# Optimization experiments

Hardware: AMD Instinct MI355X
Metric: run time of the kernel (lower is better)

Reference implementation:

```python
import jax, jax.numpy as jnp
import numpy as np

B, H, W, C = 4, 64, 64, 1024
REF_FRAC = 0.05


def setup_inputs() -> dict:
    key = jax.random.key(0)
    k1, k2 = jax.random.split(key)
    embeddings = jax.random.normal(k1, (B, H, W, C), dtype=jnp.float32)
    # sparse boolean reference masks, guaranteed non-empty per item
    ref_masks = jax.random.uniform(k2, (B, H, W)) < REF_FRAC
    ref_masks = ref_masks.at[:, 0, 0].set(True)
    return {"embeddings": embeddings, "ref_masks": ref_masks}


def reference(embeddings, ref_masks):
    """Fixed-shape JAX translation of InstanceMatcher.forward_match.

    Instead of per-item argwhere/dynamic gather, we compute the full NxN
    cosine-similarity matrix and express the ref/remaining partition with
    boolean masks. Returns:
      match  : [B, N, N] bool  -- match[b, i, j] True iff patch i is a ref patch,
               patch j is a non-ref patch, and sim > per-item median threshold
               (equivalent to the rows of the original `maps_to` output; global
               flat indices i, j map to coords via (i // W, i % W)).
      sim    : [B, N, N] float -- cosine similarities (all pairs).
      thresh : [B] float       -- median-of-max threshold per item.
    """
    Bn, Hn, Wn, Cn = embeddings.shape
    N = Hn * Wn
    x = embeddings.reshape(Bn, N, Cn)
    m = ref_masks.reshape(Bn, N)  # [B, N] bool, True = ref patch

    # F.normalize(x, dim=-1): x / max(||x||, eps)
    norm = jnp.linalg.norm(x, axis=-1, keepdims=True)
    fn = x / jnp.maximum(norm, 1e-12)

    # all-pairs cosine similarity; only (ref row, non-ref col) entries are used
    sim = jnp.einsum('bnc,bmc->bnm', fn, fn)  # [B, N, N]

    valid = m[:, :, None] & (~m)[:, None, :]  # [B, N, N]

    # max over remaining (non-ref) columns, per ref row
    max_per_ref = jnp.max(jnp.where(valid, sim, -jnp.inf), axis=2)  # [B, N]

    # torch.median (lower median) over the ref rows only: sort with non-ref
    # rows pushed to +inf, then pick element (k-1)//2 where k = #ref patches
    vals = jnp.where(m, max_per_ref, jnp.inf)
    vals_sorted = jnp.sort(vals, axis=1)
    k = jnp.sum(m, axis=1)  # [B]
    med_idx = (k - 1) // 2
    thresh = jnp.take_along_axis(vals_sorted, med_idx[:, None], axis=1)[:, 0]  # [B]

    match = valid & (sim > thresh[:, None, None])
    return match, sim, thresh
```

## Files before the change

kernel.cpp:

```cpp
#include <hip/hip_runtime.h>
#include <hip/hip_bf16.h>
#include <stdint.h>
#include <math.h>

#define BQ 4
#define NQ 4096
#define CQ 1024

#define WS_CTR      0
#define WS_THRESH   64
#define WS_MASK     256
#define WS_REFIDX   17408
#define WS_MAXV     82944
#define WS_INVN     148480
#define WS_FNB      (4u << 20)
#define WS_NEED     (WS_FNB + (32u << 20) + (1u << 20))

typedef __bf16 bf16x8 __attribute__((ext_vector_type(8)));
typedef float floatx4 __attribute__((ext_vector_type(4)));

__global__ void k_detect(const uint8_t* mraw, int* ctr) {
    int c123 = 0, c3f = 0;
    for (int i = threadIdx.x; i < BQ * NQ; i += blockDim.x) {
        uint8_t v = mraw[i];
        int m4 = i & 3;
        if (m4 != 0 && v != 0) c123++;
        if (m4 == 3 && v == 0x3F) c3f++;
    }
    atomicAdd(&ctr[0], c123);
    atomicAdd(&ctr[1], c3f);
}

__global__ void k_canon(const void* mraw, const int* ctr, uint8_t* maskc) {
    int i = blockIdx.x * blockDim.x + threadIdx.x;
    if (i >= BQ * NQ) return;
    int c123 = ctr[0], c3f = ctr[1];
    uint8_t v;
    if (c3f > 64) {
        v = (((const float*)mraw)[i] != 0.0f) ? 1 : 0;
    } else if (c123 == 0) {
        v = (((const int*)mraw)[i] != 0) ? 1 : 0;
    } else {
        v = (((const uint8_t*)mraw)[i] != 0) ? 1 : 0;
    }
    maskc[i] = v;
}

__global__ void k_compact(const uint8_t* maskc, int* refCount, int* refIdx) {
    int b = blockIdx.x;
    for (int i = threadIdx.x; i < NQ; i += blockDim.x) {
        if (maskc[b * NQ + i]) {
            int p = atomicAdd(&refCount[b], 1);
            refIdx[b * NQ + p] = i;
        }
    }
}

__global__ __launch_bounds__(128) void k_prep(const float* x, double* invn, __bf16* fnb) {
    int row = blockIdx.x;
    int t = threadIdx.x;
    const float4* xr = (const float4*)(x + (long long)row * CQ);
    float4 a = xr[t * 2 + 0];
    float4 c = xr[t * 2 + 1];
    double s = (double)a.x * a.x + (double)a.y * a.y + (double)a.z * a.z + (double)a.w * a.w
             + (double)c.x * c.x + (double)c.y * c.y + (double)c.z * c.z + (double)c.w * c.w;
    __shared__ double red[128];
    __shared__ double invs;
    red[t] = s;
    __syncthreads();
    for (int o = 64; o > 0; o >>= 1) {
        if (t < o) red[t] += red[t + o];
        __syncthreads();
    }
    if (t == 0) {
        double inv = 1.0 / fmax(sqrt(red[0]), 1e-12);
        invn[row] = inv;
        invs = inv;
    }
    __syncthreads();
    float ir = (float)invs;
    bf16x8 o8;
    o8[0] = (__bf16)(a.x * ir); o8[1] = (__bf16)(a.y * ir);
    o8[2] = (__bf16)(a.z * ir); o8[3] = (__bf16)(a.w * ir);
    o8[4] = (__bf16)(c.x * ir); o8[5] = (__bf16)(c.y * ir);
    o8[6] = (__bf16)(c.z * ir); o8[7] = (__bf16)(c.w * ir);
    *(bf16x8*)(fnb + (long long)row * CQ + t * 8) = o8;
}

#define GRID_MEGA 6144
__global__ __launch_bounds__(256) void k_mega(const __bf16* fnb, const float* x,
                                              const double* invn, const int* refCount,
                                              const int* refIdx, const uint8_t* maskc,
                                              float* sim, float* match) {
    __shared__ __align__(16) char smem[16384];
    const int t = threadIdx.x;
    const int id = blockIdx.x;

    if ((id % 3) == 2) {
        const int fid = id / 3;
        const int b = fid >> 9;
        const int rowT0 = (fid >> 6) & 7;
        const int colT = fid & 63;
        const int cnt = refCount[b];
        float* sAf = (float*)smem;
        float* sBf = (float*)(smem + 4608);
        int* sRef  = (int*)(smem + 13312);
        const float* xb = x + (long long)b * NQ * CQ;
        const int lrA = t >> 3, lkA = (t & 7) * 4;
        const int lrB = t >> 2, lkB = (t & 3) * 8;
        const int ty = t >> 4, tx = t & 15;
        for (int rowT = rowT0; rowT * 32 < cnt; rowT += 8) {
            __syncthreads();
            if (t < 32) {
                int rg = rowT * 32 + t;
                sRef[t] = (rg < cnt) ? refIdx[b * NQ + rg] : refIdx[b * NQ];
            }
            __syncthreads();
            const int arow = sRef[lrA];
            const int brow = colT * 64 + lrB;
            double acc[2][4] = {};
            for (int k0 = 0; k0 < CQ; k0 += 32) {
                float4 av = *(const float4*)(xb + (long long)arow * CQ + k0 + lkA);
                float4 b0 = *(const float4*)(xb + (long long)brow * CQ + k0 + lkB);
                float4 b1 = *(const float4*)(xb + (long long)brow * CQ + k0 + lkB + 4);
                __syncthreads();
                sAf[(lkA + 0) * 36 + lrA] = av.x; sAf[(lkA + 1) * 36 + lrA] = av.y;
                sAf[(lkA + 2) * 36 + lrA] = av.z; sAf[(lkA + 3) * 36 + lrA] = av.w;
                sBf[(lkB + 0) * 68 + lrB] = b0.x; sBf[(lkB + 1) * 68 + lrB] = b0.y;
                sBf[(lkB + 2) * 68 + lrB] = b0.z; sBf[(lkB + 3) * 68 + lrB] = b0.w;
                sBf[(lkB + 4) * 68 + lrB] = b1.x; sBf[(lkB + 5) * 68 + lrB] = b1.y;
                sBf[(lkB + 6) * 68 + lrB] = b1.z; sBf[(lkB + 7) * 68 + lrB] = b1.w;
                __syncthreads();
#pragma unroll
                for (int kk = 0; kk < 32; kk++) {
                    double a0 = (double)sAf[kk * 36 + ty * 2 + 0];
                    double a1 = (double)sAf[kk * 36 + ty * 2 + 1];
                    float4 bq = *(const float4*)(sBf + kk * 68 + tx * 4);
                    double b0d = (double)bq.x, b1d = (double)bq.y;
                    double b2d = (double)bq.z, b3d = (double)bq.w;
                    acc[0][0] += a0 * b0d; acc[0][1] += a0 * b1d;
                    acc[0][2] += a0 * b2d; acc[0][3] += a0 * b3d;
                    acc[1][0] += a1 * b0d; acc[1][1] += a1 * b1d;
                    acc[1][2] += a1 * b2d; acc[1][3] += a1 * b3d;
                }
            }
#pragma unroll
            for (int i2 = 0; i2 < 2; i2++) {
                int rg = rowT * 32 + ty * 2 + i2;
                if (rg >= cnt) continue;
                int r = sRef[ty * 2 + i2];
                double ir = invn[b * NQ + r];
#pragma unroll
                for (int j2 = 0; j2 < 4; j2++) {
                    int c = colT * 64 + tx * 4 + j2;
                    double ic = invn[b * NQ + c];
                    sim[((long long)b * NQ + r) * NQ + c] = (float)(acc[i2][j2] * ir * ic);
                }
            }
        }
    } else {
        const int gid = (id / 3) * 2 + (id % 3);
        if (gid >= 2112) return;
        const int b = gid / 528;
        int rem = gid % 528;
        int rT = 0;
        while (rem >= 32 - rT) { rem -= 32 - rT; rT++; }
        const int cT = rT + rem;
        const int rowBase = rT * 128;
        const int colBase = cT * 128;
        const __bf16* base = fnb + (long long)b * NQ * CQ;
        __bf16* smA = (__bf16*)smem;
        __bf16* smB = (__bf16*)(smem + 8192);

        const int lane = threadIdx.x & 63;
        const int w = threadIdx.x >> 6;
        const int wr = w >> 1, wc = w & 1;
        const int ldrow = lane >> 2;
        const int ldcolS = ((lane & 3) * 8) ^ (((lane >> 3) & 3) << 3);
        const int co = ((lane >> 4) * 8) ^ (((lane >> 1) & 3) << 3);

        floatx4 acc[4][4] = {};

        for (int k0 = 0; k0 < CQ; k0 += 32) {
            __syncthreads();
#pragma unroll
            for (int i = 0; i < 2; i++) {
                int rsub = w * 16 + i * 64;
                const __bf16* gA = base + (long long)(rowBase + rsub + ldrow) * CQ + k0 + ldcolS;
                const __bf16* gB = base + (long long)(colBase + rsub + ldrow) * CQ + k0 + ldcolS;
                __builtin_amdgcn_global_load_lds(
                    (const __attribute__((address_space(1))) void*)gA,
                    (__attribute__((address_space(3))) void*)(smA + rsub * 32), 16, 0, 0);
                __builtin_amdgcn_global_load_lds(
                    (const __attribute__((address_space(1))) void*)gB,
                    (__attribute__((address_space(3))) void*)(smB + rsub * 32), 16, 0, 0);
            }
            __syncthreads();

            bf16x8 af[4], bfv[4];
#pragma unroll
            for (int i = 0; i < 4; i++) {
                af[i]  = *(const bf16x8*)(smA + (wr * 64 + i * 16 + (lane & 15)) * 32 + co);
                bfv[i] = *(const bf16x8*)(smB + (wc * 64 + i * 16 + (lane & 15)) * 32 + co);
            }
#pragma unroll
            for (int i = 0; i < 4; i++)
#pragma unroll
                for (int j = 0; j < 4; j++)
                    acc[i][j] = __builtin_amdgcn_mfma_f32_16x16x32_bf16(af[i], bfv[j], acc[i][j], 0, 0, 0);
        }

        float* simb = sim + (long long)b * NQ * NQ;
        float* matb = match + (long long)b * NQ * NQ;
        const uint8_t* mrow = maskc + b * NQ;
#pragma unroll
        for (int i = 0; i < 4; i++) {
            int r0 = rowBase + wr * 64 + i * 16 + (lane >> 4) * 4;
#pragma unroll
            for (int r = 0; r < 4; r++) {
                bool isRef = mrow[r0 + r] != 0;
#pragma unroll
                for (int j = 0; j < 4; j++) {
                    int c = colBase + wc * 64 + j * 16 + (lane & 15);
                    if (!isRef) simb[(long long)(r0 + r) * NQ + c] = acc[i][j][r];
                    matb[(long long)(r0 + r) * NQ + c] = 0.0f;
                }
            }
        }

        if (rT != cT) {
            floatx4 zero4 = {0.0f, 0.0f, 0.0f, 0.0f};
#pragma unroll
            for (int i = 0; i < 4; i++) {
                int r0 = rowBase + wr * 64 + i * 16 + (lane >> 4) * 4;
#pragma unroll
                for (int j = 0; j < 4; j++) {
                    int c = colBase + wc * 64 + j * 16 + (lane & 15);
                    long long off = (long long)c * NQ + r0;
                    if (!mrow[c]) *(floatx4*)(simb + off) = acc[i][j];
                    *(floatx4*)(matb + off) = zero4;
                }
            }
        }
    }
}

__global__ __launch_bounds__(256) void k_rowmax(const float* sim, const uint8_t* maskc,
                                                const int* refCount, const int* refIdx,
                                                float* maxv) {
    int b = blockIdx.y;
    int cnt = refCount[b];
    __shared__ float red[256];
    for (int slot = blockIdx.x; slot < cnt; slot += gridDim.x) {
        int row = refIdx[b * NQ + slot];
        const float* rp = sim + ((long long)b * NQ + row) * NQ;
        float mx = -INFINITY;
        for (int j = threadIdx.x; j < NQ; j += 256) {
            if (!maskc[b * NQ + j]) mx = fmaxf(mx, rp[j]);
        }
        __syncthreads();
        red[threadIdx.x] = mx;
        __syncthreads();
        for (int o = 128; o > 0; o >>= 1) {
            if (threadIdx.x < o) red[threadIdx.x] = fmaxf(red[threadIdx.x], red[threadIdx.x + o]);
            __syncthreads();
        }
        if (threadIdx.x == 0) maxv[b * NQ + slot] = red[0];
    }
}

__global__ __launch_bounds__(256) void k_median(const float* maxv, const int* refCount,
                                                float* threshv, float* outth) {
    int b = blockIdx.x;
    int k = refCount[b];
    __shared__ float vals[NQ];
    __shared__ float result;
    for (int i = threadIdx.x; i < k; i += blockDim.x) vals[i] = maxv[b * NQ + i];
    __syncthreads();
    int med = (k - 1) / 2;
    for (int t0 = threadIdx.x; t0 < k; t0 += blockDim.x) {
        float v = vals[t0];
        int cl = 0, ce = 0;
        for (int j = 0; j < k; j++) {
            float w = vals[j];
            cl += (w < v) ? 1 : 0;
            ce += (w == v) ? 1 : 0;
        }
        if (cl <= med && med < cl + ce) result = v;
    }
    __syncthreads();
    if (threadIdx.x == 0) {
        threshv[b] = result;
        outth[b] = result;
    }
}

__global__ __launch_bounds__(256) void k_match(const float* sim, const uint8_t* maskc,
                                               const int* refCount, const int* refIdx,
                                               const float* threshv, float* match) {
    int b = blockIdx.y;
    int cnt = refCount[b];
    float th = threshv[b];
    const uint8_t* mb = maskc + b * NQ;
    for (int slot = blockIdx.x; slot < cnt; slot += gridDim.x) {
        int row = refIdx[b * NQ + slot];
        const float* rp = sim + ((long long)b * NQ + row) * NQ;
        float* op = match + ((long long)b * NQ + row) * NQ;
        for (int j = threadIdx.x * 4; j < NQ; j += 256 * 4) {
            float4 s = *(const float4*)(rp + j);
            float4 o;
            o.x = (!mb[j + 0] && s.x > th) ? 1.0f : 0.0f;
            o.y = (!mb[j + 1] && s.y > th) ? 1.0f : 0.0f;
            o.z = (!mb[j + 2] && s.z > th) ? 1.0f : 0.0f;
            o.w = (!mb[j + 3] && s.w > th) ? 1.0f : 0.0f;
            *(float4*)(op + j) = o;
        }
    }
}

extern "C" void kernel_launch(void* const* d_in, const int* in_sizes, int n_in,
                              void* d_out, int out_size, void* d_ws, size_t ws_size,
                              hipStream_t stream) {
    if (in_sizes[0] != BQ * NQ * CQ) return;
    if (ws_size < WS_NEED) return;

    const float* x = (const float*)d_in[0];
    const void* mraw = d_in[1];
    float* out = (float*)d_out;
    uint8_t* ws = (uint8_t*)d_ws;

    int* ctr       = (int*)(ws + WS_CTR);
    int* refCount  = (int*)(ws + 16);
    float* threshv = (float*)(ws + WS_THRESH);
    uint8_t* maskc = ws + WS_MASK;
    int* refIdx    = (int*)(ws + WS_REFIDX);
    float* maxv    = (float*)(ws + WS_MAXV);
    double* invn   = (double*)(ws + WS_INVN);
    __bf16* fnb    = (__bf16*)(ws + WS_FNB);

    float* match = out;
    float* sim   = out + (long long)BQ * NQ * NQ;
    float* outth = out + 2LL * BQ * NQ * NQ;

    hipMemsetAsync(ws, 0, 4096, stream);

    k_detect<<<1, 256, 0, stream>>>((const uint8_t*)mraw, ctr);
    k_canon<<<(BQ * NQ + 255) / 256, 256, 0, stream>>>(mraw, ctr, maskc);
    k_compact<<<BQ, 256, 0, stream>>>(maskc, refCount, refIdx);
    k_prep<<<BQ * NQ, 128, 0, stream>>>(x, invn, fnb);
    k_mega<<<GRID_MEGA, 256, 0, stream>>>(fnb, x, invn, refCount, refIdx, maskc, sim, match);
    k_rowmax<<<dim3(256, BQ), 256, 0, stream>>>(sim, maskc, refCount, refIdx, maxv);
    k_median<<<BQ, 256, 0, stream>>>(maxv, refCount, threshv, outth);
    k_match<<<dim3(256, BQ), 256, 0, stream>>>(sim, maskc, refCount, refIdx, threshv, match);
}
```

Measured before the change: 996.1 us.

## Replace fp64 ref-row GEMM with split-bf16 (hi/lo) MFMA for all tiles

Drops the separate FP64 SIMT path that recomputed ref rows at high precision. The normalized embeddings are now stored as a bf16 hi/lo pair, and every tile is computed with four bf16 MFMAs (hi*hi, hi*lo, lo*hi, lo*lo) to get near-fp32 accuracy. The grid is reduced to just the symmetric GEMM tiles, with a batch-interleaved block ordering. This removes the slow scalar double-precision work but quadruples the MFMA count and doubles the operand traffic, and results are no longer fp64-exact for the ref rows used in the threshold.

Result: faster. 845.9 us (-15.1%).

```diff
diff --git a/kernel.cpp b/kernel.cpp
--- a/kernel.cpp
+++ b/kernel.cpp
@@ -12,9 +12,9 @@
 #define WS_MASK     256
 #define WS_REFIDX   17408
 #define WS_MAXV     82944
-#define WS_INVN     148480
-#define WS_FNB      (4u << 20)
-#define WS_NEED     (WS_FNB + (32u << 20) + (1u << 20))
+#define WS_FNH      (4u << 20)
+#define WS_FNL      (WS_FNH + (32u << 20))
+#define WS_NEED     (WS_FNL + (32u << 20) + (1u << 20))
 
 typedef __bf16 bf16x8 __attribute__((ext_vector_type(8)));
 typedef float floatx4 __attribute__((ext_vector_type(4)));
@@ -56,7 +56,7 @@
     }
 }
 
-__global__ __launch_bounds__(128) void k_prep(const float* x, double* invn, __bf16* fnb) {
+__global__ __launch_bounds__(128) void k_prep(const float* x, __bf16* fnh, __bf16* fnl) {
     int row = blockIdx.x;
     int t = threadIdx.x;
     const float4* xr = (const float4*)(x + (long long)row * CQ);
@@ -72,174 +72,121 @@
         if (t < o) red[t] += red[t + o];
         __syncthreads();
     }
-    if (t == 0) {
-        double inv = 1.0 / fmax(sqrt(red[0]), 1e-12);
-        invn[row] = inv;
-        invs = inv;
-    }
+    if (t == 0) invs = 1.0 / fmax(sqrt(red[0]), 1e-12);
     __syncthreads();
     float ir = (float)invs;
-    bf16x8 o8;
-    o8[0] = (__bf16)(a.x * ir); o8[1] = (__bf16)(a.y * ir);
-    o8[2] = (__bf16)(a.z * ir); o8[3] = (__bf16)(a.w * ir);
-    o8[4] = (__bf16)(c.x * ir); o8[5] = (__bf16)(c.y * ir);
-    o8[6] = (__bf16)(c.z * ir); o8[7] = (__bf16)(c.w * ir);
-    *(bf16x8*)(fnb + (long long)row * CQ + t * 8) = o8;
-}
-
-#define GRID_MEGA 6144
-__global__ __launch_bounds__(256) void k_mega(const __bf16* fnb, const float* x,
-                                              const double* invn, const int* refCount,
-                                              const int* refIdx, const uint8_t* maskc,
+    float v[8] = {a.x, a.y, a.z, a.w, c.x, c.y, c.z, c.w};
+    bf16x8 h8, l8;
+#pragma unroll
+    for (int j = 0; j < 8; j++) {
+        float xn = v[j] * ir;
+        __bf16 h = (__bf16)xn;
+        h8[j] = h;
+        l8[j] = (__bf16)(xn - (float)h);
+    }
+    *(bf16x8*)(fnh + (long long)row * CQ + t * 8) = h8;
+    *(bf16x8*)(fnl + (long long)row * CQ + t * 8) = l8;
+}
+
+#define GRID_MEGA 2112
+__global__ __launch_bounds__(256) void k_mega(const __bf16* fnh, const __bf16* fnl,
                                               float* sim, float* match) {
-    __shared__ __align__(16) char smem[16384];
-    const int t = threadIdx.x;
+    __shared__ __align__(16) char smem[32768];
     const int id = blockIdx.x;
-
-    if ((id % 3) == 2) {
-        const int fid = id / 3;
-        const int b = fid >> 9;
-        const int rowT0 = (fid >> 6) & 7;
-        const int colT = fid & 63;
-        const int cnt = refCount[b];
-        float* sAf = (float*)smem;
-        float* sBf = (float*)(smem + 4608);
-        int* sRef  = (int*)(smem + 13312);
-        const float* xb = x + (long long)b * NQ * CQ;
-        const int lrA = t >> 3, lkA = (t & 7) * 4;
-        const int lrB = t >> 2, lkB = (t & 3) * 8;
-        const int ty = t >> 4, tx = t & 15;
-        for (int rowT = rowT0; rowT * 32 < cnt; rowT += 8) {
-            __syncthreads();
-            if (t < 32) {
-                int rg = rowT * 32 + t;
-                sRef[t] = (rg < cnt) ? refIdx[b * NQ + rg] : refIdx[b * NQ];
+    const int gid = (id & 7) * 264 + (id >> 3);
+    const int b = gid / 528;
+    int rem = gid % 528;
+    int rT = 0;
+    while (rem >= 32 - rT) { rem -= 32 - rT; rT++; }
+    const int cT = rT + rem;
+    const int rowBase = rT * 128;
+    const int colBase = cT * 128;
+    const __bf16* baseh = fnh + (long long)b * NQ * CQ;
+    const __bf16* basel = fnl + (long long)b * NQ * CQ;
+    __bf16* smAh = (__bf16*)smem;
+    __bf16* smAl = (__bf16*)(smem + 8192);
+    __bf16* smBh = (__bf16*)(smem + 16384);
+    __bf16* smBl = (__bf16*)(smem + 24576);
+
+    const int lane = threadIdx.x & 63;
+    const int w = threadIdx.x >> 6;
+    const int wr = w >> 1, wc = w & 1;
+    const int ldrow = lane >> 2;
+    const int ldcolS = ((lane & 3) * 8) ^ (((lane >> 3) & 3) << 3);
+    const int co = ((lane >> 4) * 8) ^ (((lane >> 1) & 3) << 3);
+
+    floatx4 acc[4][4] = {};
+
+    for (int k0 = 0; k0 < CQ; k0 += 32) {
+        __syncthreads();
+#pragma unroll
+        for (int i = 0; i < 2; i++) {
+            int rsub = w * 16 + i * 64;
+            long long offA = (long long)(rowBase + rsub + ldrow) * CQ + k0 + ldcolS;
+            long long offB = (long long)(colBase + rsub + ldrow) * CQ + k0 + ldcolS;
+            __builtin_amdgcn_global_load_lds(
+                (const __attribute__((address_space(1))) void*)(baseh + offA),
+                (__attribute__((address_space(3))) void*)(smAh + rsub * 32), 16, 0, 0);
+            __builtin_amdgcn_global_load_lds(
+                (const __attribute__((address_space(1))) void*)(basel + offA),
+                (__attribute__((address_space(3))) void*)(smAl + rsub * 32), 16, 0, 0);
+            __builtin_amdgcn_global_load_lds(
+                (const __attribute__((address_space(1))) void*)(baseh + offB),
+                (__attribute__((address_space(3))) void*)(smBh + rsub * 32), 16, 0, 0);
+            __builtin_amdgcn_global_load_lds(
+                (const __attribute__((address_space(1))) void*)(basel + offB),
+                (__attribute__((address_space(3))) void*)(smBl + rsub * 32), 16, 0, 0);
+        }
+        __syncthreads();
+
+        bf16x8 ah[4], al[4];
+#pragma unroll
+        for (int i = 0; i < 4; i++) {
+            int ra = (wr * 64 + i * 16 + (lane & 15)) * 32 + co;
+            ah[i] = *(const bf16x8*)(smAh + ra);
+            al[i] = *(const bf16x8*)(smAl + ra);
+        }
+#pragma unroll
+        for (int j = 0; j < 4; j++) {
+            int rb = (wc * 64 + j * 16 + (lane & 15)) * 32 + co;
+            bf16x8 bh = *(const bf16x8*)(smBh + rb);
+            bf16x8 bl = *(const bf16x8*)(smBl + rb);
+#pragma unroll
+            for (int i = 0; i < 4; i++) {
+                acc[i][j] = __builtin_amdgcn_mfma_f32_16x16x32_bf16(ah[i], bh, acc[i][j], 0, 0, 0);
+                acc[i][j] = __builtin_amdgcn_mfma_f32_16x16x32_bf16(ah[i], bl, acc[i][j], 0, 0, 0);
+                acc[i][j] = __builtin_amdgcn_mfma_f32_16x16x32_bf16(al[i], bh, acc[i][j], 0, 0, 0);
+                acc[i][j] = __builtin_amdgcn_mfma_f32_16x16x32_bf16(al[i], bl, acc[i][j], 0, 0, 0);
             }
-            __syncthreads();
-            const int arow = sRef[lrA];
-            const int brow = colT * 64 + lrB;
-            double acc[2][4] = {};
-            for (int k0 = 0; k0 < CQ; k0 += 32) {
-                float4 av = *(const float4*)(xb + (long long)arow * CQ + k0 + lkA);
-                float4 b0 = *(const float4*)(xb + (long long)brow * CQ + k0 + lkB);
-                float4 b1 = *(const float4*)(xb + (long long)brow * CQ + k0 + lkB + 4);
-                __syncthreads();
-                sAf[(lkA + 0) * 36 + lrA] = av.x; sAf[(lkA + 1) * 36 + lrA] = av.y;
-                sAf[(lkA + 2) * 36 + lrA] = av.z; sAf[(lkA + 3) * 36 + lrA] = av.w;
-                sBf[(lkB + 0) * 68 + lrB] = b0.x; sBf[(lkB + 1) * 68 + lrB] = b0.y;
-                sBf[(lkB + 2) * 68 + lrB] = b0.z; sBf[(lkB + 3) * 68 + lrB] = b0.w;
-                sBf[(lkB + 4) * 68 + lrB] = b1.x; sBf[(lkB + 5) * 68 + lrB] = b1.y;
-                sBf[(lkB + 6) * 68 + lrB] = b1.z; sBf[(lkB + 7) * 68 + lrB] = b1.w;
-                __syncthreads();
-#pragma unroll
-                for (int kk = 0; kk < 32; kk++) {
-                    double a0 = (double)sAf[kk * 36 + ty * 2 + 0];
-                    double a1 = (double)sAf[kk * 36 + ty * 2 + 1];
-                    float4 bq = *(const float4*)(sBf + kk * 68 + tx * 4);
-                    double b0d = (double)bq.x, b1d = (double)bq.y;
-                    double b2d = (double)bq.z, b3d = (double)bq.w;
-                    acc[0][0] += a0 * b0d; acc[0][1] += a0 * b1d;
-                    acc[0][2] += a0 * b2d; acc[0][3] += a0 * b3d;
-                    acc[1][0] += a1 * b0d; acc[1][1] += a1 * b1d;
-                    acc[1][2] += a1 * b2d; acc[1][3] += a1 * b3d;
-                }
+        }
+    }
+
+    float* simb = sim + (long long)b * NQ * NQ;
+    float* matb = match + (long long)b * NQ * NQ;
+#pragma unroll
+    for (int i = 0; i < 4; i++) {
+        int r0 = rowBase + wr * 64 + i * 16 + (lane >> 4) * 4;
+#pragma unroll
+        for (int r = 0; r < 4; r++) {
+#pragma unroll
+            for (int j = 0; j < 4; j++) {
+                int c = colBase + wc * 64 + j * 16 + (lane & 15);
+                simb[(long long)(r0 + r) * NQ + c] = acc[i][j][r];
+                matb[(long long)(r0 + r) * NQ + c] = 0.0f;
             }
-#pragma unroll
-            for (int i2 = 0; i2 < 2; i2++) {
-                int rg = rowT * 32 + ty * 2 + i2;
-                if (rg >= cnt) continue;
-                int r = sRef[ty * 2 + i2];
-                double ir = invn[b * NQ + r];
-#pragma unroll
-                for (int j2 = 0; j2 < 4; j2++) {
-                    int c = colT * 64 + tx * 4 + j2;
-                    double ic = invn[b * NQ + c];
-                    sim[((long long)b * NQ + r) * NQ + c] = (float)(acc[i2][j2] * ir * ic);
-                }
-            }
-        }
-    } else {
-        const int gid = (id / 3) * 2 + (id % 3);
-        if (gid >= 2112) return;
-        const int b = gid / 528;
-        int rem = gid % 528;
-        int rT = 0;
-        while (rem >= 32 - rT) { rem -= 32 - rT; rT++; }
-        const int cT = rT + rem;
-        const int rowBase = rT * 128;
-        const int colBase = cT * 128;
-        const __bf16* base = fnb + (long long)b * NQ * CQ;
-        __bf16* smA = (__bf16*)smem;
-        __bf16* smB = (__bf16*)(smem + 8192);
-
-        const int lane = threadIdx.x & 63;
-        const int w = threadIdx.x >> 6;
-        const int wr = w >> 1, wc = w & 1;
-        const int ldrow = lane >> 2;
-        const int ldcolS = ((lane & 3) * 8) ^ (((lane >> 3) & 3) << 3);
-        const int co = ((lane >> 4) * 8) ^ (((lane >> 1) & 3) << 3);
-
-        floatx4 acc[4][4] = {};
-
-        for (int k0 = 0; k0 < CQ; k0 += 32) {
-            __syncthreads();
-#pragma unroll
-            for (int i = 0; i < 2; i++) {
-                int rsub = w * 16 + i * 64;
-                const __bf16* gA = base + (long long)(rowBase + rsub + ldrow) * CQ + k0 + ldcolS;
-                const __bf16* gB = base + (long long)(colBase + rsub + ldrow) * CQ + k0 + ldcolS;
-                __builtin_amdgcn_global_load_lds(
-                    (const __attribute__((address_space(1))) void*)gA,
-                    (__attribute__((address_space(3))) void*)(smA + rsub * 32), 16, 0, 0);
-                __builtin_amdgcn_global_load_lds(
-                    (const __attribute__((address_space(1))) void*)gB,
-                    (__attribute__((address_space(3))) void*)(smB + rsub * 32), 16, 0, 0);
-            }
-            __syncthreads();
-
-            bf16x8 af[4], bfv[4];
-#pragma unroll
-            for (int i = 0; i < 4; i++) {
-                af[i]  = *(const bf16x8*)(smA + (wr * 64 + i * 16 + (lane & 15)) * 32 + co);
-                bfv[i] = *(const bf16x8*)(smB + (wc * 64 + i * 16 + (lane & 15)) * 32 + co);
-            }
-#pragma unroll
-            for (int i = 0; i < 4; i++)
-#pragma unroll
-                for (int j = 0; j < 4; j++)
-                    acc[i][j] = __builtin_amdgcn_mfma_f32_16x16x32_bf16(af[i], bfv[j], acc[i][j], 0, 0, 0);
-        }
-
-        float* simb = sim + (long long)b * NQ * NQ;
-        float* matb = match + (long long)b * NQ * NQ;
-        const uint8_t* mrow = maskc + b * NQ;
+        }
+    }
+    if (rT != cT) {
+        floatx4 zero4 = {0.0f, 0.0f, 0.0f, 0.0f};
 #pragma unroll
         for (int i = 0; i < 4; i++) {
             int r0 = rowBase + wr * 64 + i * 16 + (lane >> 4) * 4;
 #pragma unroll
-            for (int r = 0; r < 4; r++) {
-                bool isRef = mrow[r0 + r] != 0;
-#pragma unroll
-                for (int j = 0; j < 4; j++) {
-                    int c = colBase + wc * 64 + j * 16 + (lane & 15);
-                    if (!isRef) simb[(long long)(r0 + r) * NQ + c] = acc[i][j][r];
-                    matb[(long long)(r0 + r) * NQ + c] = 0.0f;
-                }
-            }
-        }
-
-        if (rT != cT) {
-            floatx4 zero4 = {0.0f, 0.0f, 0.0f, 0.0f};
-#pragma unroll
-            for (int i = 0; i < 4; i++) {
-                int r0 = rowBase + wr * 64 + i * 16 + (lane >> 4) * 4;
-#pragma unroll
-                for (int j = 0; j < 4; j++) {
-                    int c = colBase + wc * 64 + j * 16 + (lane & 15);
-                    long long off = (long long)c * NQ + r0;
-                    if (!mrow[c]) *(floatx4*)(simb + off) = acc[i][j];
-                    *(floatx4*)(matb + off) = zero4;
-                }
+            for (int j = 0; j < 4; j++) {
+                int c = colBase + wc * 64 + j * 16 + (lane & 15);
+                long long off = (long long)c * NQ + r0;
+                *(floatx4*)(simb + off) = acc[i][j];
+                *(floatx4*)(matb + off) = zero4;
             }
         }
     }
@@ -335,8 +282,8 @@
     uint8_t* maskc = ws + WS_MASK;
     int* refIdx    = (int*)(ws + WS_REFIDX);
     float* maxv    = (float*)(ws + WS_MAXV);
-    double* invn   = (double*)(ws + WS_INVN);
-    __bf16* fnb    = (__bf16*)(ws + WS_FNB);
+    __bf16* fnh    = (__bf16*)(ws + WS_FNH);
+    __bf16* fnl    = (__bf16*)(ws + WS_FNL);
 
     float* match = out;
     float* sim   = out + (long long)BQ * NQ * NQ;
@@ -347,8 +294,8 @@
     k_detect<<<1, 256, 0, stream>>>((const uint8_t*)mraw, ctr);
     k_canon<<<(BQ * NQ + 255) / 256, 256, 0, stream>>>(mraw, ctr, maskc);
     k_compact<<<BQ, 256, 0, stream>>>(maskc, refCount, refIdx);
-    k_prep<<<BQ * NQ, 128, 0, stream>>>(x, invn, fnb);
-    k_mega<<<GRID_MEGA, 256, 0, stream>>>(fnb, x, invn, refCount, refIdx, maskc, sim, match);
+    k_prep<<<BQ * NQ, 128, 0, stream>>>(x, fnh, fnl);
+    k_mega<<<GRID_MEGA, 256, 0, stream>>>(fnh, fnl, sim, match);
     k_rowmax<<<dim3(256, BQ), 256, 0, stream>>>(sim, maskc, refCount, refIdx, maxv);
     k_median<<<BQ, 256, 0, stream>>>(maxv, refCount, threshv, outth);
     k_match<<<dim3(256, BQ), 256, 0, stream>>>(sim, maskc, refCount, refIdx, threshv, match);
```
